# Optimization experiments

Hardware: AMD Instinct MI355X
Metric: run time of the kernel (lower is better)

## Reference

```python
import jax, jax.numpy as jnp
import numpy as np
import math

B, T, S, C, H = 2, 2048, 576, 1024, 16
D = C // H
EPS = 1e-5


def _ln(x, w, b):
    m = jnp.mean(x, axis=-1, keepdims=True)
    v = jnp.mean((x - m) ** 2, axis=-1, keepdims=True)
    return (x - m) * jax.lax.rsqrt(v + EPS) * w + b


def setup_inputs() -> dict:
    key = jax.random.key(0)
    ks = jax.random.split(key, 20)
    s = 0.02
    return {
        "x": jax.random.normal(ks[0], (B, T, C), jnp.float32),
        "context": jax.random.normal(ks[1], (B, S, C), jnp.float32),
        "ln1_w": jnp.ones((C,), jnp.float32), "ln1_b": jnp.zeros((C,), jnp.float32),
        "ln2_w": jnp.ones((C,), jnp.float32), "ln2_b": jnp.zeros((C,), jnp.float32),
        "ln3_w": jnp.ones((C,), jnp.float32), "ln3_b": jnp.zeros((C,), jnp.float32),
        "attn_wqkv": jax.random.normal(ks[2], (C, 3 * C), jnp.float32) * s,
        "attn_bqkv": jnp.zeros((3 * C,), jnp.float32),
        "attn_wproj": jax.random.normal(ks[3], (C, C), jnp.float32) * s,
        "attn_bproj": jnp.zeros((C,), jnp.float32),
        "ca_wq": jax.random.normal(ks[4], (C, C), jnp.float32) * s,
        "ca_bq": jnp.zeros((C,), jnp.float32),
        "ca_wk": jax.random.normal(ks[5], (C, C), jnp.float32) * s,
        "ca_bk": jnp.zeros((C,), jnp.float32),
        "ca_wv": jax.random.normal(ks[6], (C, C), jnp.float32) * s,
        "ca_bv": jnp.zeros((C,), jnp.float32),
        "ca_wproj": jax.random.normal(ks[7], (C, C), jnp.float32) * s,
        "ca_bproj": jnp.zeros((C,), jnp.float32),
        "fc_w": jax.random.normal(ks[8], (C, 4 * C), jnp.float32) * s,
        "fc_b": jnp.zeros((4 * C,), jnp.float32),
        "proj_w": jax.random.normal(ks[9], (4 * C, C), jnp.float32) * s,
        "proj_b": jnp.zeros((C,), jnp.float32),
    }


def reference(x, context, ln1_w, ln1_b, ln2_w, ln2_b, ln3_w, ln3_b,
              attn_wqkv, attn_bqkv, attn_wproj, attn_bproj,
              ca_wq, ca_bq, ca_wk, ca_bk, ca_wv, ca_bv, ca_wproj, ca_bproj,
              fc_w, fc_b, proj_w, proj_b):
    b, t, c = x.shape
    scale = 1.0 / math.sqrt(D)

    # --- causal self-attention ---
    h = _ln(x, ln1_w, ln1_b)
    qkv = h @ attn_wqkv + attn_bqkv                       # [B,T,3C]
    q, k, v = jnp.split(qkv, 3, axis=-1)
    q = q.reshape(b, t, H, D).transpose(0, 2, 1, 3)       # [B,H,T,D]
    k = k.reshape(b, t, H, D).transpose(0, 2, 1, 3)
    v = v.reshape(b, t, H, D).transpose(0, 2, 1, 3)
    att = jnp.einsum('bhqd,bhkd->bhqk', q, k) * scale     # [B,H,T,T]
    causal = jnp.tril(jnp.ones((t, t), dtype=bool))
    att = jnp.where(causal, att, -jnp.inf)
    att = jax.nn.softmax(att, axis=-1)
    sa = jnp.einsum('bhqk,bhkd->bhqd', att, v).transpose(0, 2, 1, 3).reshape(b, t, c)
    x = x + sa @ attn_wproj + attn_bproj

    # --- cross-attention ---
    h = _ln(x, ln2_w, ln2_b)
    s = context.shape[1]
    q = (h @ ca_wq + ca_bq).reshape(b, t, H, D).transpose(0, 2, 1, 3)        # [B,H,T,D]
    k = (context @ ca_wk + ca_bk).reshape(b, s, H, D).transpose(0, 2, 1, 3)  # [B,H,S,D]
    v = (context @ ca_wv + ca_bv).reshape(b, s, H, D).transpose(0, 2, 1, 3)
    scores = jnp.einsum('bhqd,bhkd->bhqk', q, k) * scale                      # [B,H,T,S]
    attn_prob = jax.nn.softmax(scores, axis=-1)
    ca = jnp.einsum('bhqk,bhkd->bhqd', attn_prob, v).transpose(0, 2, 1, 3).reshape(b, t, c)
    x = x + ca @ ca_wproj + ca_bproj

    # --- GELU(tanh) MLP ---
    h = _ln(x, ln3_w, ln3_b)
    h = jax.nn.gelu(h @ fc_w + fc_b, approximate=True)
    x = x + h @ proj_w + proj_b
    return x, attn_prob
```

## Files before the change

### kernel.cpp

```cpp
#include <hip/hip_runtime.h>

typedef __bf16 bf16_t;
typedef __attribute__((ext_vector_type(8))) __bf16 bf16x8;
typedef __attribute__((ext_vector_type(4))) __bf16 bf16x4;
typedef __attribute__((ext_vector_type(4))) float f32x4;

static constexpr int kB = 2, kT = 2048, kS = 576, kC = 1024, kH = 16, kD = 64;

#define MFMA16(a, b, c) __builtin_amdgcn_mfma_f32_16x16x32_bf16((a), (b), (c), 0, 0, 0)

__device__ __forceinline__ void gld_lds16(const bf16_t* g, bf16_t* l) {
    __builtin_amdgcn_global_load_lds((const __attribute__((address_space(1))) unsigned int*)g,
                                     (__attribute__((address_space(3))) unsigned int*)l, 16, 0, 0);
}

__device__ inline float gelu_tanh(float x) {
    float u = 1.5957691216057308f * (x + 0.044715f * x * x * x);
    float t = 1.f - 2.f / (__expf(u) + 1.f);
    return 0.5f * x * (1.f + t);
}

__global__ void transpose_w(const float* __restrict__ W, bf16_t* __restrict__ WT, int K, int N) {
    __shared__ float tile[32][33];
    int n0 = blockIdx.x * 32, k0 = blockIdx.y * 32;
    int tx = threadIdx.x, ty = threadIdx.y;
#pragma unroll
    for (int i = 0; i < 4; ++i)
        tile[ty + i * 8][tx] = W[(size_t)(k0 + ty + i * 8) * N + n0 + tx];
    __syncthreads();
#pragma unroll
    for (int i = 0; i < 4; ++i)
        WT[(size_t)(n0 + ty + i * 8) * K + k0 + tx] = (bf16_t)tile[tx][ty + i * 8];
}

__global__ void f32_to_bf16(const float* __restrict__ in, bf16_t* __restrict__ out, int n4) {
    int i = blockIdx.x * 256 + threadIdx.x;
    if (i < n4) {
        float4 v = ((const float4*)in)[i];
        bf16x4 o;
        o[0] = (bf16_t)v.x; o[1] = (bf16_t)v.y; o[2] = (bf16_t)v.z; o[3] = (bf16_t)v.w;
        ((bf16x4*)out)[i] = o;
    }
}

__global__ __launch_bounds__(256) void ln_kernel(const float* __restrict__ x,
                                                 const float* __restrict__ w,
                                                 const float* __restrict__ bb,
                                                 bf16_t* __restrict__ out) {
    int row = blockIdx.x, tid = threadIdx.x;
    const float* xr = x + (size_t)row * kC;
    float4 v = ((const float4*)xr)[tid];
    float s1 = v.x + v.y + v.z + v.w;
    float s2 = v.x * v.x + v.y * v.y + v.z * v.z + v.w * v.w;
#pragma unroll
    for (int o = 32; o > 0; o >>= 1) {
        s1 += __shfl_down(s1, o);
        s2 += __shfl_down(s2, o);
    }
    __shared__ float red[8];
    __shared__ float mv[2];
    int wid = tid >> 6, lane = tid & 63;
    if (lane == 0) { red[wid] = s1; red[4 + wid] = s2; }
    __syncthreads();
    if (tid == 0) {
        float a = red[0] + red[1] + red[2] + red[3];
        float c = red[4] + red[5] + red[6] + red[7];
        float mean = a * (1.f / kC);
        float var = c * (1.f / kC) - mean * mean;
        mv[0] = mean;
        mv[1] = rsqrtf(var + 1e-5f);
    }
    __syncthreads();
    float mean = mv[0], rstd = mv[1];
    float4 wv = ((const float4*)w)[tid];
    float4 bv = ((const float4*)bb)[tid];
    bf16x4 o4;
    o4[0] = (bf16_t)((v.x - mean) * rstd * wv.x + bv.x);
    o4[1] = (bf16_t)((v.y - mean) * rstd * wv.y + bv.y);
    o4[2] = (bf16_t)((v.z - mean) * rstd * wv.z + bv.z);
    o4[3] = (bf16_t)((v.w - mean) * rstd * wv.w + bv.w);
    *(bf16x4*)&out[(size_t)row * kC + tid * 4] = o4;
}

template <int EPI, int BM>
__global__ __launch_bounds__(256) void gemm128(const bf16_t* __restrict__ A, const bf16_t* __restrict__ Bw,
                                               const float* __restrict__ bias, const float* __restrict__ res,
                                               void* __restrict__ Out, void* __restrict__ Out2,
                                               void* __restrict__ Out3, int M, int N, int K, int lda, int ldb,
                                               int ldc) {
    constexpr int MT = BM / 32;
    constexpr int ASZ = BM * 64, BSZ = 128 * 64;
    __shared__ __align__(16) bf16_t As[2 * ASZ];
    __shared__ __align__(16) bf16_t Bs[2 * BSZ];
    const int tid = threadIdx.x;
    const int m0 = blockIdx.y * BM, n0 = blockIdx.x * 128;
    const int lane = tid & 63, wid = tid >> 6;
    const int l16 = lane & 15, quad = lane >> 4;
    const int wm = (wid >> 1) * (BM / 2), wn = (wid & 1) * 64;
    f32x4 acc[MT][4] = {};

    const bf16_t* Ab = A + (size_t)m0 * lda;
    const bf16_t* Bb = Bw + (size_t)n0 * ldb;

    auto stage = [&](int buf, int k0) {
#pragma unroll
        for (int i = 0; i < BM / 32; ++i) {
            int chunk = tid + i * 256;
            int row = chunk >> 3, col = (chunk & 7) * 8;
            gld_lds16(Ab + (size_t)row * lda + k0 + col, As + buf * ASZ + row * 64 + col);
        }
#pragma unroll
        for (int i = 0; i < 4; ++i) {
            int chunk = tid + i * 256;
            int row = chunk >> 3, col = (chunk & 7) * 8;
            gld_lds16(Bb + (size_t)row * ldb + k0 + col, Bs + buf * BSZ + row * 64 + col);
        }
    };

    const int nk = K / 64;
    stage(0, 0);
    int cur = 0;
    for (int t = 0; t < nk; ++t) {
        __syncthreads();
        if (t + 1 < nk) stage(cur ^ 1, (t + 1) * 64);
#pragma unroll
        for (int kk = 0; kk < 64; kk += 32) {
            bf16x8 af[MT], bw[4];
#pragma unroll
            for (int mt = 0; mt < MT; ++mt)
                af[mt] = *(const bf16x8*)&As[cur * ASZ + (wm + mt * 16 + l16) * 64 + kk + quad * 8];
#pragma unroll
            for (int nt = 0; nt < 4; ++nt)
                bw[nt] = *(const bf16x8*)&Bs[cur * BSZ + (wn + nt * 16 + l16) * 64 + kk + quad * 8];
#pragma unroll
            for (int mt = 0; mt < MT; ++mt)
#pragma unroll
                for (int nt = 0; nt < 4; ++nt) acc[mt][nt] = MFMA16(af[mt], bw[nt], acc[mt][nt]);
        }
        cur ^= 1;
    }

#pragma unroll
    for (int mt = 0; mt < MT; ++mt)
#pragma unroll
        for (int nt = 0; nt < 4; ++nt) {
            int n = n0 + wn + nt * 16 + l16;
            float bv = bias ? bias[n] : 0.f;
#pragma unroll
            for (int r = 0; r < 4; ++r) {
                int m = m0 + wm + mt * 16 + quad * 4 + r;
                float v = acc[mt][nt][r] + bv;
                if constexpr (EPI == 2) v = gelu_tanh(v);
                if constexpr (EPI == 0 || EPI == 2) {
                    ((bf16_t*)Out)[(size_t)m * ldc + n] = (bf16_t)v;
                } else if constexpr (EPI == 1) {
                    ((float*)Out)[(size_t)m * ldc + n] = v + res[(size_t)m * ldc + n];
                } else {
                    int b = m >> 11, t = m & 2047;
                    if (n < 2048) {
                        int h = (n & 1023) >> 6, d = n & 63;
                        bf16_t* dst = (n < 1024) ? (bf16_t*)Out : (bf16_t*)Out2;
                        dst[(((size_t)b * kH + h) * kT + t) * kD + d] = (bf16_t)v;
                    } else {
                        int n2 = n - 2048;
                        int h = n2 >> 6, d = n2 & 63;
                        ((bf16_t*)Out3)[(((size_t)b * kH + h) * kD + d) * kT + t] = (bf16_t)v;
                    }
                }
            }
        }
}

__global__ __launch_bounds__(256) void flash_self3(const bf16_t* __restrict__ qb, const bf16_t* __restrict__ kb,
                                                   const bf16_t* __restrict__ vT, bf16_t* __restrict__ sa) {
    const int tid = threadIdx.x;
    const int qi = gridDim.x - 1 - blockIdx.x;
    const int h = blockIdx.y, b = blockIdx.z;
    const int lane = tid & 63, wid = tid >> 6;
    const int l16 = lane & 15, quad = lane >> 4;
    const size_t bh = (size_t)b * kH + h;

    __shared__ __align__(16) bf16_t Qs[64 * 64];
    __shared__ __align__(16) bf16_t Ks[64 * 64];
    __shared__ __align__(16) bf16_t VTs[64 * 64];
    bf16_t* Ps = Qs;

    const bf16_t* qsrc = qb + (bh * kT + (size_t)qi * 64) * kD;
#pragma unroll
    for (int i = 0; i < 2; ++i) {
        int chunk = tid + i * 256;
        gld_lds16(qsrc + chunk * 8, Qs + chunk * 8);
    }
    __syncthreads();
    bf16x8 aq[2];
    aq[0] = *(const bf16x8*)&Qs[(wid * 16 + l16) * 64 + quad * 8];
    aq[1] = *(const bf16x8*)&Qs[(wid * 16 + l16) * 64 + 32 + quad * 8];
#pragma unroll
    for (int j = 0; j < 8; ++j) { aq[0][j] *= (bf16_t)0.125f; aq[1][j] *= (bf16_t)0.125f; }

    f32x4 o[4] = {};
    float lsum[4] = {0.f, 0.f, 0.f, 0.f};
    const int qrow = qi * 64 + wid * 16 + quad * 4;

    for (int kt = 0; kt <= qi; ++kt) {
        __syncthreads();
        const bf16_t* ksrc = kb + (bh * kT + (size_t)kt * 64) * kD;
        const bf16_t* vsrc = vT + bh * kD * kT + (size_t)kt * 64;
#pragma unroll
        for (int i = 0; i < 2; ++i) {
            int chunk = tid + i * 256;
            gld_lds16(ksrc + chunk * 8, Ks + chunk * 8);
            int row = chunk >> 3, col = (chunk & 7) * 8;
            gld_lds16(vsrc + (size_t)row * kT + col, VTs + chunk * 16ull / 2);
        }
        __syncthreads();

        f32x4 sf[4] = {};
#pragma unroll
        for (int kk = 0; kk < 2; ++kk)
#pragma unroll
            for (int nt = 0; nt < 4; ++nt) {
                bf16x8 bk = *(const bf16x8*)&Ks[(nt * 16 + l16) * 64 + kk * 32 + quad * 8];
                sf[nt] = MFMA16(aq[kk], bk, sf[nt]);
            }

        const bool diag = (kt == qi);
#pragma unroll
        for (int nt = 0; nt < 4; ++nt) {
            int col = kt * 64 + nt * 16 + l16;
#pragma unroll
            for (int r = 0; r < 4; ++r) {
                float s = sf[nt][r];
                if (diag && col > qrow + r) s = -1e30f;
                float p = __expf(s);
                lsum[r] += p;
                Ps[(wid * 16 + quad * 4 + r) * 64 + nt * 16 + l16] = (bf16_t)p;
            }
        }
#pragma unroll
        for (int kk = 0; kk < 2; ++kk) {
            bf16x8 ap = *(const bf16x8*)&Ps[(wid * 16 + l16) * 64 + kk * 32 + quad * 8];
#pragma unroll
            for (int dt = 0; dt < 4; ++dt) {
                bf16x8 bv = *(const bf16x8*)&VTs[(dt * 16 + l16) * 64 + kk * 32 + quad * 8];
                o[dt] = MFMA16(ap, bv, o[dt]);
            }
        }
    }

#pragma unroll
    for (int r = 0; r < 4; ++r) {
        float s = lsum[r];
#pragma unroll
        for (int off = 1; off < 16; off <<= 1) s += __shfl_xor(s, off, 16);
        float inv = 1.f / s;
        size_t row = (size_t)b * kT + qi * 64 + wid * 16 + quad * 4 + r;
#pragma unroll
        for (int dt = 0; dt < 4; ++dt)
            sa[row * kC + h * kD + dt * 16 + l16] = (bf16_t)(o[dt][r] * inv);
    }
}

__global__ __launch_bounds__(256) void ca_fused(const bf16_t* __restrict__ q2, const bf16_t* __restrict__ k2,
                                                const bf16_t* __restrict__ v2T, bf16_t* __restrict__ ca,
                                                float* __restrict__ probs) {
    const int tid = threadIdx.x;
    const int qi = blockIdx.x, z = blockIdx.y;
    const int b = z >> 4, h = z & 15;
    const int lane = tid & 63, wid = tid >> 6;
    const int l16 = lane & 15, quad = lane >> 4;
    const size_t bh = (size_t)z;

    __shared__ __align__(16) bf16_t Qs[64 * 64];
    __shared__ __align__(16) bf16_t Ks[64 * 64];
    __shared__ __align__(16) bf16_t VTs[64 * 64];
    bf16_t* Ps = Qs;

#pragma unroll
    for (int i = 0; i < 2; ++i) {
        int chunk = tid + i * 256;
        int row = chunk >> 3, col = (chunk & 7) * 8;
        gld_lds16(q2 + ((size_t)(b * kT + qi * 64 + row)) * kC + h * kD + col, Qs + chunk * 8);
    }
    __syncthreads();
    bf16x8 aq[2];
    aq[0] = *(const bf16x8*)&Qs[(wid * 16 + l16) * 64 + quad * 8];
    aq[1] = *(const bf16x8*)&Qs[(wid * 16 + l16) * 64 + 32 + quad * 8];
#pragma unroll
    for (int j = 0; j < 8; ++j) { aq[0][j] *= (bf16_t)0.125f; aq[1][j] *= (bf16_t)0.125f; }

    f32x4 o[4] = {};
    float lsum[4] = {0.f, 0.f, 0.f, 0.f};
    bf16x4 pk[9][4];

#pragma unroll
    for (int kt = 0; kt < 9; ++kt) {
        __syncthreads();
#pragma unroll
        for (int i = 0; i < 2; ++i) {
            int chunk = tid + i * 256;
            int row = chunk >> 3, col = (chunk & 7) * 8;
            gld_lds16(k2 + ((size_t)(b * kS + kt * 64 + row)) * kC + h * kD + col, Ks + chunk * 8);
            gld_lds16(v2T + (bh * kD + row) * kS + kt * 64 + col, VTs + chunk * 8);
        }
        __syncthreads();

        f32x4 sf[4] = {};
#pragma unroll
        for (int kk = 0; kk < 2; ++kk)
#pragma unroll
            for (int nt = 0; nt < 4; ++nt) {
                bf16x8 bk = *(const bf16x8*)&Ks[(nt * 16 + l16) * 64 + kk * 32 + quad * 8];
                sf[nt] = MFMA16(aq[kk], bk, sf[nt]);
            }
#pragma unroll
        for (int nt = 0; nt < 4; ++nt) {
            bf16x4 pc;
#pragma unroll
            for (int r = 0; r < 4; ++r) {
                float p = __expf(sf[nt][r]);
                lsum[r] += p;
                bf16_t pb = (bf16_t)p;
                pc[r] = pb;
                Ps[(wid * 16 + quad * 4 + r) * 64 + nt * 16 + l16] = pb;
            }
            pk[kt][nt] = pc;
        }
#pragma unroll
        for (int kk = 0; kk < 2; ++kk) {
            bf16x8 ap = *(const bf16x8*)&Ps[(wid * 16 + l16) * 64 + kk * 32 + quad * 8];
#pragma unroll
            for (int dt = 0; dt < 4; ++dt) {
                bf16x8 bv = *(const bf16x8*)&VTs[(dt * 16 + l16) * 64 + kk * 32 + quad * 8];
                o[dt] = MFMA16(ap, bv, o[dt]);
            }
        }
    }

    float inv[4];
#pragma unroll
    for (int r = 0; r < 4; ++r) {
        float s = lsum[r];
#pragma unroll
        for (int off = 1; off < 16; off <<= 1) s += __shfl_xor(s, off, 16);
        inv[r] = 1.f / s;
        size_t row = (size_t)b * kT + qi * 64 + wid * 16 + quad * 4 + r;
#pragma unroll
        for (int dt = 0; dt < 4; ++dt)
            ca[row * kC + h * kD + dt * 16 + l16] = (bf16_t)(o[dt][r] * inv[r]);
    }
#pragma unroll
    for (int r = 0; r < 4; ++r) {
        float* dst = probs + ((size_t)z * kT + qi * 64 + wid * 16 + quad * 4 + r) * kS;
#pragma unroll
        for (int kt = 0; kt < 9; ++kt)
#pragma unroll
            for (int nt = 0; nt < 4; ++nt)
                dst[kt * 64 + nt * 16 + l16] = (float)pk[kt][nt][r] * inv[r];
    }
}

__global__ void v_transpose(const bf16_t* __restrict__ v2, bf16_t* __restrict__ v2T) {
    int idx = blockIdx.x * 256 + threadIdx.x;
    int s = idx % kS;
    int t = idx / kS;
    int d = t % kD; t /= kD;
    int h = t % kH;
    int b = t / kH;
    v2T[idx] = v2[((size_t)(b * kS + s)) * kC + h * kD + d];
}

extern "C" void kernel_launch(void* const* d_in, const int* in_sizes, int n_in, void* d_out, int out_size,
                              void* d_ws, size_t ws_size, hipStream_t stream) {
    const float* x = (const float*)d_in[0];
    const float* context = (const float*)d_in[1];
    const float* ln1_w = (const float*)d_in[2];
    const float* ln1_b = (const float*)d_in[3];
    const float* ln2_w = (const float*)d_in[4];
    const float* ln2_b = (const float*)d_in[5];
    const float* ln3_w = (const float*)d_in[6];
    const float* ln3_b = (const float*)d_in[7];
    const float* attn_wqkv = (const float*)d_in[8];
    const float* attn_bqkv = (const float*)d_in[9];
    const float* attn_wproj = (const float*)d_in[10];
    const float* attn_bproj = (const float*)d_in[11];
    const float* ca_wq = (const float*)d_in[12];
    const float* ca_bq = (const float*)d_in[13];
    const float* ca_wk = (const float*)d_in[14];
    const float* ca_bk = (const float*)d_in[15];
    const float* ca_wv = (const float*)d_in[16];
    const float* ca_bv = (const float*)d_in[17];
    const float* ca_wproj = (const float*)d_in[18];
    const float* ca_bproj = (const float*)d_in[19];
    const float* fc_w = (const float*)d_in[20];
    const float* fc_b = (const float*)d_in[21];
    const float* proj_w = (const float*)d_in[22];
    const float* proj_b = (const float*)d_in[23];

    float* out_x = (float*)d_out;
    float* probs = out_x + (size_t)kB * kT * kC;

    char* wsp = (char*)d_ws;
    size_t off = 0;
    auto alloc = [&](size_t bytes) -> void* {
        void* p = wsp + off;
        off += (bytes + 255) & ~(size_t)255;
        return p;
    };
    bf16_t* wT_qkv   = (bf16_t*)alloc((size_t)3 * kC * kC * 2);
    bf16_t* wT_aproj = (bf16_t*)alloc((size_t)kC * kC * 2);
    bf16_t* wT_caq   = (bf16_t*)alloc((size_t)kC * kC * 2);
    bf16_t* wT_cak   = (bf16_t*)alloc((size_t)kC * kC * 2);
    bf16_t* wT_cav   = (bf16_t*)alloc((size_t)kC * kC * 2);
    bf16_t* wT_caproj= (bf16_t*)alloc((size_t)kC * kC * 2);
    bf16_t* wT_fc    = (bf16_t*)alloc((size_t)4 * kC * kC * 2);
    bf16_t* wT_proj  = (bf16_t*)alloc((size_t)4 * kC * kC * 2);
    bf16_t* hbuf     = (bf16_t*)alloc((size_t)kB * kT * kC * 2);
    bf16_t* qb       = (bf16_t*)alloc((size_t)kB * kT * kC * 2);
    bf16_t* kbuf     = (bf16_t*)alloc((size_t)kB * kT * kC * 2);
    bf16_t* vTb      = (bf16_t*)alloc((size_t)kB * kT * kC * 2);
    bf16_t* sabuf    = (bf16_t*)alloc((size_t)kB * kT * kC * 2);
    float*  x1       = (float*)alloc((size_t)kB * kT * kC * 4);
    float*  x2       = (float*)alloc((size_t)kB * kT * kC * 4);
    bf16_t* ctxb     = (bf16_t*)alloc((size_t)kB * kS * kC * 2);
    bf16_t* q2       = (bf16_t*)alloc((size_t)kB * kT * kC * 2);
    bf16_t* k2       = (bf16_t*)alloc((size_t)kB * kS * kC * 2);
    bf16_t* v2       = (bf16_t*)alloc((size_t)kB * kS * kC * 2);
    bf16_t* v2T      = (bf16_t*)alloc((size_t)kB * kS * kC * 2);
    bf16_t* hf       = (bf16_t*)alloc((size_t)kB * kT * 4 * kC * 2);
    (void)ws_size;

    dim3 tb(32, 8);
    transpose_w<<<dim3(96, 32), tb, 0, stream>>>(attn_wqkv, wT_qkv, kC, 3 * kC);
    transpose_w<<<dim3(32, 32), tb, 0, stream>>>(attn_wproj, wT_aproj, kC, kC);
    transpose_w<<<dim3(32, 32), tb, 0, stream>>>(ca_wq, wT_caq, kC, kC);
    transpose_w<<<dim3(32, 32), tb, 0, stream>>>(ca_wk, wT_cak, kC, kC);
    transpose_w<<<dim3(32, 32), tb, 0, stream>>>(ca_wv, wT_cav, kC, kC);
    transpose_w<<<dim3(32, 32), tb, 0, stream>>>(ca_wproj, wT_caproj, kC, kC);
    transpose_w<<<dim3(128, 32), tb, 0, stream>>>(fc_w, wT_fc, kC, 4 * kC);
    transpose_w<<<dim3(32, 128), tb, 0, stream>>>(proj_w, wT_proj, 4 * kC, kC);
    f32_to_bf16<<<dim3((kB * kS * kC / 4 + 255) / 256), 256, 0, stream>>>(context, ctxb, kB * kS * kC / 4);

    const int Mtok = kB * kT;
    ln_kernel<<<Mtok, 256, 0, stream>>>(x, ln1_w, ln1_b, hbuf);
    gemm128<4, 128><<<dim3(24, 32), 256, 0, stream>>>(hbuf, wT_qkv, attn_bqkv, nullptr, qb, kbuf, vTb, Mtok,
                                                      3 * kC, kC, kC, kC, 0);
    flash_self3<<<dim3(kT / 64, kH, kB), 256, 0, stream>>>(qb, kbuf, vTb, sabuf);
    gemm128<1, 64><<<dim3(8, 64), 256, 0, stream>>>(sabuf, wT_aproj, attn_bproj, x, x1, nullptr, nullptr, Mtok,
                                                    kC, kC, kC, kC, kC);
    ln_kernel<<<Mtok, 256, 0, stream>>>(x1, ln2_w, ln2_b, hbuf);
    gemm128<0, 64><<<dim3(8, 64), 256, 0, stream>>>(hbuf, wT_caq, ca_bq, nullptr, q2, nullptr, nullptr, Mtok, kC,
                                                    kC, kC, kC, kC);
    gemm128<0, 64><<<dim3(8, 18), 256, 0, stream>>>(ctxb, wT_cak, ca_bk, nullptr, k2, nullptr, nullptr, kB * kS,
                                                    kC, kC, kC, kC, kC);
    gemm128<0, 64><<<dim3(8, 18), 256, 0, stream>>>(ctxb, wT_cav, ca_bv, nullptr, v2, nullptr, nullptr, kB * kS,
                                                    kC, kC, kC, kC, kC);
    v_transpose<<<dim3(kB * kH * kD * kS / 256), 256, 0, stream>>>(v2, v2T);
    ca_fused<<<dim3(kT / 64, kB * kH), 256, 0, stream>>>(q2, k2, v2T, sabuf, probs);
    gemm128<1, 64><<<dim3(8, 64), 256, 0, stream>>>(sabuf, wT_caproj, ca_bproj, x1, x2, nullptr, nullptr, Mtok,
                                                    kC, kC, kC, kC, kC);
    ln_kernel<<<Mtok, 256, 0, stream>>>(x2, ln3_w, ln3_b, hbuf);
    gemm128<2, 128><<<dim3(32, 32), 256, 0, stream>>>(hbuf, wT_fc, fc_b, nullptr, hf, nullptr, nullptr, Mtok,
                                                      4 * kC, kC, kC, kC, 4 * kC);
    gemm128<1, 64><<<dim3(8, 64), 256, 0, stream>>>(hf, wT_proj, proj_b, x2, out_x, nullptr, nullptr, Mtok, kC,
                                                    4 * kC, 4 * kC, 4 * kC, kC);
}
```

Baseline: 773.6 us.

## Double-buffer K/V tiles and XOR-swizzle LDS in both attention kernels

Both the causal self-attention and the cross-attention kernels now keep two LDS buffers for K and V^T. The next tile is prefetched with global_load_lds while the current tile is consumed, which drops one barrier per iteration and overlaps global loads with MFMA work. LDS tiles for Q, K, V^T and P now use an XOR swizzle on the 16-byte chunk index, applied through the global source addresses and the matching read and write indices, to cut LDS bank conflicts. The cost is more LDS per block, which may lower occupancy.

```diff
diff --git a/kernel.cpp b/kernel.cpp
--- a/kernel.cpp
+++ b/kernel.cpp
@@ -13,6 +13,8 @@
     __builtin_amdgcn_global_load_lds((const __attribute__((address_space(1))) unsigned int*)g,
                                      (__attribute__((address_space(3))) unsigned int*)l, 16, 0, 0);
 }
+
+__device__ __forceinline__ int swz(int row, int q) { return row * 64 + (((q ^ (row & 7)) & 7) << 3); }
 
 __device__ inline float gelu_tanh(float x) {
     float u = 1.5957691216057308f * (x + 0.044715f * x * x * x);
@@ -171,7 +173,7 @@
         }
 }
 
-__global__ __launch_bounds__(256) void flash_self3(const bf16_t* __restrict__ qb, const bf16_t* __restrict__ kb,
+__global__ __launch_bounds__(256) void flash_self4(const bf16_t* __restrict__ qb, const bf16_t* __restrict__ kb,
                                                    const bf16_t* __restrict__ vT, bf16_t* __restrict__ sa) {
     const int tid = threadIdx.x;
     const int qi = gridDim.x - 1 - blockIdx.x;
@@ -179,48 +181,60 @@
     const int lane = tid & 63, wid = tid >> 6;
     const int l16 = lane & 15, quad = lane >> 4;
     const size_t bh = (size_t)b * kH + h;
-
-    __shared__ __align__(16) bf16_t Qs[64 * 64];
-    __shared__ __align__(16) bf16_t Ks[64 * 64];
-    __shared__ __align__(16) bf16_t VTs[64 * 64];
+    constexpr int TSZ = 64 * 64;
+
+    __shared__ __align__(16) bf16_t Qs[TSZ];
+    __shared__ __align__(16) bf16_t Ks[2 * TSZ];
+    __shared__ __align__(16) bf16_t VTs[2 * TSZ];
     bf16_t* Ps = Qs;
 
     const bf16_t* qsrc = qb + (bh * kT + (size_t)qi * 64) * kD;
+    const bf16_t* kbase = kb + bh * kT * kD;
+    const bf16_t* vbase = vT + bh * kD * kT;
+
 #pragma unroll
     for (int i = 0; i < 2; ++i) {
         int chunk = tid + i * 256;
-        gld_lds16(qsrc + chunk * 8, Qs + chunk * 8);
-    }
+        int row = chunk >> 3, c8 = chunk & 7;
+        gld_lds16(qsrc + row * 64 + ((c8 ^ (row & 7)) << 3), Qs + chunk * 8);
+    }
+
+    auto stageKV = [&](int buf, int kt) {
+        const bf16_t* ksrc = kbase + (size_t)kt * 64 * kD;
+        const bf16_t* vsrc = vbase + (size_t)kt * 64;
+#pragma unroll
+        for (int i = 0; i < 2; ++i) {
+            int chunk = tid + i * 256;
+            int row = chunk >> 3, c8 = chunk & 7;
+            int sc = (c8 ^ (row & 7)) << 3;
+            gld_lds16(ksrc + row * 64 + sc, Ks + buf * TSZ + chunk * 8);
+            gld_lds16(vsrc + (size_t)row * kT + sc, VTs + buf * TSZ + chunk * 8);
+        }
+    };
+    stageKV(0, 0);
+
     __syncthreads();
     bf16x8 aq[2];
-    aq[0] = *(const bf16x8*)&Qs[(wid * 16 + l16) * 64 + quad * 8];
-    aq[1] = *(const bf16x8*)&Qs[(wid * 16 + l16) * 64 + 32 + quad * 8];
+    aq[0] = *(const bf16x8*)&Qs[swz(wid * 16 + l16, quad)];
+    aq[1] = *(const bf16x8*)&Qs[swz(wid * 16 + l16, 4 + quad)];
 #pragma unroll
     for (int j = 0; j < 8; ++j) { aq[0][j] *= (bf16_t)0.125f; aq[1][j] *= (bf16_t)0.125f; }
 
     f32x4 o[4] = {};
     float lsum[4] = {0.f, 0.f, 0.f, 0.f};
     const int qrow = qi * 64 + wid * 16 + quad * 4;
+    int cur = 0;
 
     for (int kt = 0; kt <= qi; ++kt) {
-        __syncthreads();
-        const bf16_t* ksrc = kb + (bh * kT + (size_t)kt * 64) * kD;
-        const bf16_t* vsrc = vT + bh * kD * kT + (size_t)kt * 64;
-#pragma unroll
-        for (int i = 0; i < 2; ++i) {
-            int chunk = tid + i * 256;
-            gld_lds16(ksrc + chunk * 8, Ks + chunk * 8);
-            int row = chunk >> 3, col = (chunk & 7) * 8;
-            gld_lds16(vsrc + (size_t)row * kT + col, VTs + chunk * 16ull / 2);
-        }
-        __syncthreads();
+        if (kt) __syncthreads();
+        if (kt < qi) stageKV(cur ^ 1, kt + 1);
 
         f32x4 sf[4] = {};
 #pragma unroll
         for (int kk = 0; kk < 2; ++kk)
 #pragma unroll
             for (int nt = 0; nt < 4; ++nt) {
-                bf16x8 bk = *(const bf16x8*)&Ks[(nt * 16 + l16) * 64 + kk * 32 + quad * 8];
+                bf16x8 bk = *(const bf16x8*)&Ks[cur * TSZ + swz(nt * 16 + l16, kk * 4 + quad)];
                 sf[nt] = MFMA16(aq[kk], bk, sf[nt]);
             }
 
@@ -234,18 +248,21 @@
                 if (diag && col > qrow + r) s = -1e30f;
                 float p = __expf(s);
                 lsum[r] += p;
-                Ps[(wid * 16 + quad * 4 + r) * 64 + nt * 16 + l16] = (bf16_t)p;
+                int rp = wid * 16 + quad * 4 + r;
+                int cc = nt * 16 + l16;
+                Ps[rp * 64 + (cc ^ ((rp & 7) << 3))] = (bf16_t)p;
             }
         }
 #pragma unroll
         for (int kk = 0; kk < 2; ++kk) {
-            bf16x8 ap = *(const bf16x8*)&Ps[(wid * 16 + l16) * 64 + kk * 32 + quad * 8];
+            bf16x8 ap = *(const bf16x8*)&Ps[swz(wid * 16 + l16, kk * 4 + quad)];
 #pragma unroll
             for (int dt = 0; dt < 4; ++dt) {
-                bf16x8 bv = *(const bf16x8*)&VTs[(dt * 16 + l16) * 64 + kk * 32 + quad * 8];
+                bf16x8 bv = *(const bf16x8*)&VTs[cur * TSZ + swz(dt * 16 + l16, kk * 4 + quad)];
                 o[dt] = MFMA16(ap, bv, o[dt]);
             }
         }
+        cur ^= 1;
     }
 
 #pragma unroll
@@ -270,47 +287,56 @@
     const int lane = tid & 63, wid = tid >> 6;
     const int l16 = lane & 15, quad = lane >> 4;
     const size_t bh = (size_t)z;
-
-    __shared__ __align__(16) bf16_t Qs[64 * 64];
-    __shared__ __align__(16) bf16_t Ks[64 * 64];
-    __shared__ __align__(16) bf16_t VTs[64 * 64];
+    constexpr int TSZ = 64 * 64;
+
+    __shared__ __align__(16) bf16_t Qs[TSZ];
+    __shared__ __align__(16) bf16_t Ks[2 * TSZ];
+    __shared__ __align__(16) bf16_t VTs[2 * TSZ];
     bf16_t* Ps = Qs;
 
 #pragma unroll
     for (int i = 0; i < 2; ++i) {
         int chunk = tid + i * 256;
-        int row = chunk >> 3, col = (chunk & 7) * 8;
-        gld_lds16(q2 + ((size_t)(b * kT + qi * 64 + row)) * kC + h * kD + col, Qs + chunk * 8);
-    }
+        int row = chunk >> 3, c8 = chunk & 7;
+        gld_lds16(q2 + ((size_t)(b * kT + qi * 64 + row)) * kC + h * kD + ((c8 ^ (row & 7)) << 3),
+                  Qs + chunk * 8);
+    }
+
+    auto stageKV = [&](int buf, int kt) {
+#pragma unroll
+        for (int i = 0; i < 2; ++i) {
+            int chunk = tid + i * 256;
+            int row = chunk >> 3, c8 = chunk & 7;
+            int sc = (c8 ^ (row & 7)) << 3;
+            gld_lds16(k2 + ((size_t)(b * kS + kt * 64 + row)) * kC + h * kD + sc, Ks + buf * TSZ + chunk * 8);
+            gld_lds16(v2T + (bh * kD + row) * kS + kt * 64 + sc, VTs + buf * TSZ + chunk * 8);
+        }
+    };
+    stageKV(0, 0);
+
     __syncthreads();
     bf16x8 aq[2];
-    aq[0] = *(const bf16x8*)&Qs[(wid * 16 + l16) * 64 + quad * 8];
-    aq[1] = *(const bf16x8*)&Qs[(wid * 16 + l16) * 64 + 32 + quad * 8];
+    aq[0] = *(const bf16x8*)&Qs[swz(wid * 16 + l16, quad)];
+    aq[1] = *(const bf16x8*)&Qs[swz(wid * 16 + l16, 4 + quad)];
 #pragma unroll
     for (int j = 0; j < 8; ++j) { aq[0][j] *= (bf16_t)0.125f; aq[1][j] *= (bf16_t)0.125f; }
 
     f32x4 o[4] = {};
     float lsum[4] = {0.f, 0.f, 0.f, 0.f};
     bf16x4 pk[9][4];
+    int cur = 0;
 
 #pragma unroll
     for (int kt = 0; kt < 9; ++kt) {
-        __syncthreads();
-#pragma unroll
-        for (int i = 0; i < 2; ++i) {
-            int chunk = tid + i * 256;
-            int row = chunk >> 3, col = (chunk & 7) * 8;
-            gld_lds16(k2 + ((size_t)(b * kS + kt * 64 + row)) * kC + h * kD + col, Ks + chunk * 8);
-            gld_lds16(v2T + (bh * kD + row) * kS + kt * 64 + col, VTs + chunk * 8);
-        }
-        __syncthreads();
+        if (kt) __syncthreads();
+        if (kt < 8) stageKV(cur ^ 1, kt + 1);
 
         f32x4 sf[4] = {};
 #pragma unroll
         for (int kk = 0; kk < 2; ++kk)
 #pragma unroll
             for (int nt = 0; nt < 4; ++nt) {
-                bf16x8 bk = *(const bf16x8*)&Ks[(nt * 16 + l16) * 64 + kk * 32 + quad * 8];
+                bf16x8 bk = *(const bf16x8*)&Ks[cur * TSZ + swz(nt * 16 + l16, kk * 4 + quad)];
                 sf[nt] = MFMA16(aq[kk], bk, sf[nt]);
             }
 #pragma unroll
@@ -322,19 +348,22 @@
                 lsum[r] += p;
                 bf16_t pb = (bf16_t)p;
                 pc[r] = pb;
-                Ps[(wid * 16 + quad * 4 + r) * 64 + nt * 16 + l16] = pb;
+                int rp = wid * 16 + quad * 4 + r;
+                int cc = nt * 16 + l16;
+                Ps[rp * 64 + (cc ^ ((rp & 7) << 3))] = pb;
             }
             pk[kt][nt] = pc;
         }
 #pragma unroll
         for (int kk = 0; kk < 2; ++kk) {
-            bf16x8 ap = *(const bf16x8*)&Ps[(wid * 16 + l16) * 64 + kk * 32 + quad * 8];
+            bf16x8 ap = *(const bf16x8*)&Ps[swz(wid * 16 + l16, kk * 4 + quad)];
 #pragma unroll
             for (int dt = 0; dt < 4; ++dt) {
-                bf16x8 bv = *(const bf16x8*)&VTs[(dt * 16 + l16) * 64 + kk * 32 + quad * 8];
+                bf16x8 bv = *(const bf16x8*)&VTs[cur * TSZ + swz(dt * 16 + l16, kk * 4 + quad)];
                 o[dt] = MFMA16(ap, bv, o[dt]);
             }
         }
+        cur ^= 1;
     }
 
     float inv[4];
@@ -445,7 +474,7 @@
     ln_kernel<<<Mtok, 256, 0, stream>>>(x, ln1_w, ln1_b, hbuf);
     gemm128<4, 128><<<dim3(24, 32), 256, 0, stream>>>(hbuf, wT_qkv, attn_bqkv, nullptr, qb, kbuf, vTb, Mtok,
                                                       3 * kC, kC, kC, kC, 0);
-    flash_self3<<<dim3(kT / 64, kH, kB), 256, 0, stream>>>(qb, kbuf, vTb, sabuf);
+    flash_self4<<<dim3(kT / 64, kH, kB), 256, 0, stream>>>(qb, kbuf, vTb, sabuf);
     gemm128<1, 64><<<dim3(8, 64), 256, 0, stream>>>(sabuf, wT_aproj, attn_bproj, x, x1, nullptr, nullptr, Mtok,
                                                     kC, kC, kC, kC, kC);
     ln_kernel<<<Mtok, 256, 0, stream>>>(x1, ln2_w, ln2_b, hbuf);
```

Measured after the change: 762.5 us. No clear change (-1.4%).
